# Kernel optimization log

Measured on AMD Instinct MI355X. Metric: run time of the kernel, lower is better.

The kernel has to match this reference:

```python
import jax, jax.numpy as jnp
import numpy as np

N = 20000       # num_nodes
E = 200000      # ~ N*N*0.0005 directed edges from erdos_renyi
IN = 64         # in_channels
HID = 128       # hidden_channels (per head)
H = 4           # heads
OUT = 10        # out_channels
K1 = 10000      # ceil(0.5*N) nodes kept by pool1 (single graph -> static)
K2 = 5000       # ceil(0.5*K1) kept by pool2
NEG_SLOPE = 0.2 # PyG GATConv default negative_slope


def setup_inputs() -> dict:
    key = jax.random.key(0)
    ks = jax.random.split(key, 16)
    def glorot(k, shp, fan):
        return (jax.random.normal(k, shp, jnp.float32) / np.sqrt(fan)).astype(jnp.float32)
    x = jax.random.normal(ks[0], (N, IN), jnp.float32)
    edge_index = jax.random.randint(ks[1], (2, E), 0, N, dtype=jnp.int32)
    batch = jnp.zeros((N,), jnp.int32)
    W1 = glorot(ks[2], (IN, H * HID), IN)
    a_src1 = glorot(ks[3], (H, HID), HID)
    a_dst1 = glorot(ks[4], (H, HID), HID)
    b1 = jnp.zeros((H * HID,), jnp.float32)
    pw1 = glorot(ks[5], (H * HID,), H * HID)
    W2 = glorot(ks[6], (H * HID, H * HID), H * HID)
    a_src2 = glorot(ks[7], (H, HID), HID)
    a_dst2 = glorot(ks[8], (H, HID), HID)
    b2 = jnp.zeros((H * HID,), jnp.float32)
    pw2 = glorot(ks[9], (H * HID,), H * HID)
    Wl = glorot(ks[10], (H * HID, OUT), H * HID)
    bl = jnp.zeros((OUT,), jnp.float32)
    return dict(x=x, edge_index=edge_index, batch=batch,
                W1=W1, a_src1=a_src1, a_dst1=a_dst1, b1=b1, pw1=pw1,
                W2=W2, a_src2=a_src2, a_dst2=a_dst2, b2=b2, pw2=pw2,
                Wl=Wl, bl=bl)


def _gat(x, src, dst, emask, W, a_src, a_dst, bias):
    """PyG GATConv: gather -> LeakyReLU edge score -> scatter-softmax over dst -> scatter-add.
    Self-loops added (PyG default). emask marks valid edges (invalid edges point at node 0)."""
    n = x.shape[0]
    Hh, C = a_src.shape
    h = (x @ W).reshape(n, Hh, C)                      # [n,H,C]
    asrc = jnp.einsum('nhc,hc->nh', h, a_src)          # [n,H]
    adst = jnp.einsum('nhc,hc->nh', h, a_dst)
    loops = jnp.arange(n, dtype=src.dtype)
    sa = jnp.concatenate([src, loops])                 # [E+n]
    da = jnp.concatenate([dst, loops])
    ma = jnp.concatenate([emask, jnp.ones((n,), bool)])
    logit = jax.nn.leaky_relu(asrc[sa] + adst[da], negative_slope=NEG_SLOPE)  # [E+n,H]
    logit = jnp.where(ma[:, None], logit, -1e9)
    mx = jax.ops.segment_max(logit, da, num_segments=n)        # every node has a self-loop
    e = jnp.where(ma[:, None], jnp.exp(logit - mx[da]), 0.0)
    den = jax.ops.segment_sum(e, da, num_segments=n)
    alpha = e / den[da]                                         # [E+n,H]
    msg = (alpha[:, :, None] * h[sa]).reshape(-1, Hh * C)       # [E+n,H*C]
    return jax.ops.segment_sum(msg, da, num_segments=n) + bias  # concat heads + bias


def _topk_pool(x, src, dst, emask, w, k):
    """PyG TopKPooling (single graph): score = tanh(x.w/||w||), keep top-k nodes,
    scale kept features by score, relabel & mask edges between kept nodes."""
    score = jnp.tanh((x @ w) / jnp.linalg.norm(w))     # [n]
    vals, perm = jax.lax.top_k(score, k)
    xn = x[perm] * vals[:, None]                       # [k,F]
    remap = jnp.full((x.shape[0],), -1, jnp.int32).at[perm].set(jnp.arange(k, dtype=jnp.int32))
    s2 = remap[src]
    d2 = remap[dst]
    m2 = emask & (s2 >= 0) & (d2 >= 0)
    return xn, jnp.where(m2, s2, 0), jnp.where(m2, d2, 0), m2


def reference(x, edge_index, batch, W1, a_src1, a_dst1, b1, pw1,
              W2, a_src2, a_dst2, b2, pw2, Wl, bl):
    src = edge_index[0]
    dst = edge_index[1]
    mask = jnp.ones((src.shape[0],), bool)
    h = jax.nn.elu(_gat(x, src, dst, mask, W1, a_src1, a_dst1, b1))
    h, src, dst, mask = _topk_pool(h, src, dst, mask, pw1, K1)
    h = jax.nn.elu(_gat(h, src, dst, mask, W2, a_src2, a_dst2, b2))
    h, src, dst, mask = _topk_pool(h, src, dst, mask, pw2, K2)
    g = jnp.mean(h, axis=0, keepdims=True)             # global_mean_pool, single graph
    return g @ Wl + bl                                  # [1, OUT]
```

## Files before the change

kernel.cpp:

```cpp
#include <hip/hip_runtime.h>
#include <math.h>

#define N_NODES 20000
#define E_EDGES 200000
#define K1_KEEP 10000
#define K2_KEEP 5000
#define HIDC 128
#define NHEAD 4
#define FDIM 512
#define NEG 0.2f
#define BSTRIDE 64
#define SELCAP 20
#define MPAD 10112
#define MPAD1 20096
#define FR_GRID 250
#define FR_RPB 40

typedef _Float16 half8 __attribute__((ext_vector_type(8)));
typedef _Float16 half4 __attribute__((ext_vector_type(4)));
typedef float f32x4 __attribute__((ext_vector_type(4)));

__device__ __forceinline__ float leaky(float x){ return x > 0.f ? x : NEG * x; }
__device__ __forceinline__ float elu(float x){ return x > 0.f ? x : expm1f(x); }
__device__ __forceinline__ unsigned ordkey(float f){
    unsigned u = __float_as_uint(f);
    return (u & 0x80000000u) ? ~u : (u | 0x80000000u);
}

__global__ __launch_bounds__(256) void prep_x(const float* __restrict__ x,
        _Float16* __restrict__ X0, _Float16* __restrict__ X1)
{
    int tid = blockIdx.x * 256 + threadIdx.x;
    int r = tid >> 3, c8 = (tid & 7) << 3;
    half8 v0 = (half8)0, v1 = (half8)0;
    if (r < N_NODES){
        const float4* p = reinterpret_cast<const float4*>(&x[(size_t)r * 64 + c8]);
        float4 x0 = p[0], x1 = p[1];
        float vals[8] = {x0.x, x0.y, x0.z, x0.w, x1.x, x1.y, x1.z, x1.w};
#pragma unroll
        for (int j = 0; j < 8; ++j){
            _Float16 h = (_Float16)vals[j];
            v0[j] = h;
            v1[j] = (_Float16)(vals[j] - (float)h);
        }
    }
    *reinterpret_cast<half8*>(&X0[(size_t)r * 64 + c8]) = v0;
    *reinterpret_cast<half8*>(&X1[(size_t)r * 64 + c8]) = v1;
}

__global__ __launch_bounds__(256) void prep_w1x(const float* __restrict__ W1,
        _Float16* __restrict__ B0, _Float16* __restrict__ B1,
        int* __restrict__ ctmp, int cn,
        const float* __restrict__ cw, float* __restrict__ cinvn)
{
    int bid = blockIdx.x;
    int t = threadIdx.x;
    if (bid < 32){
        __shared__ float tile[32][33];
        int bn = bid & 15, bk = bid >> 4;
        int n0 = bn * 32, k0 = bk * 32;
        int j = t & 31, i0 = t >> 5;
#pragma unroll
        for (int ii = 0; ii < 32; ii += 8)
            tile[i0 + ii][j] = W1[(size_t)(k0 + i0 + ii) * 512 + n0 + j];
        __syncthreads();
#pragma unroll
        for (int ii = 0; ii < 32; ii += 8){
            float v = tile[j][i0 + ii];
            _Float16 h0 = (_Float16)v;
            _Float16 h1 = (_Float16)(v - (float)h0);
            size_t o = (size_t)(n0 + i0 + ii) * 64 + k0 + j;
            B0[o] = h0; B1[o] = h1;
        }
    } else if (bid < 32 + 79){
        int i = (bid - 32) * 256 + t;
        if (i < cn) ctmp[i] = 0;
    } else {
        __shared__ float redc[4];
        float s = cw[t] * cw[t] + cw[t + 256] * cw[t + 256];
#pragma unroll
        for (int off = 32; off > 0; off >>= 1) s += __shfl_xor(s, off);
        if ((t & 63) == 0) redc[t >> 6] = s;
        __syncthreads();
        if (t == 0) *cinvn = rsqrtf(redc[0] + redc[1] + redc[2] + redc[3]);
    }
}

__global__ __launch_bounds__(256) void prep_w2(const float* __restrict__ W2,
        _Float16* __restrict__ B0, _Float16* __restrict__ B1)
{
    __shared__ float tile[32][33];
    int bn = blockIdx.x & 15, bk = blockIdx.x >> 4;
    int n0 = bn * 32, k0 = bk * 32;
    int t = threadIdx.x;
    int j = t & 31, i0 = t >> 5;
#pragma unroll
    for (int ii = 0; ii < 32; ii += 8)
        tile[i0 + ii][j] = W2[(size_t)(k0 + i0 + ii) * 512 + n0 + j];
    __syncthreads();
#pragma unroll
    for (int ii = 0; ii < 32; ii += 8){
        float v = tile[j][i0 + ii];
        _Float16 h0 = (_Float16)v;
        _Float16 h1 = (_Float16)(v - (float)h0);
        size_t o = (size_t)(n0 + i0 + ii) * 512 + k0 + j;
        B0[o] = h0; B1[o] = h1;
    }
}

__global__ __launch_bounds__(256) void prep_a(const float* __restrict__ out1,
        const int* __restrict__ oldi, const float* __restrict__ score,
        _Float16* __restrict__ A0, _Float16* __restrict__ A1)
{
    int tid = blockIdx.x * 256 + threadIdx.x;
    int r = tid >> 6, kq = (tid & 63) << 3;
    half8 v0 = (half8)0, v1 = (half8)0;
    if (r < K1_KEEP){
        int o = oldi[r];
        float sc = score[o];
        const float4* p = reinterpret_cast<const float4*>(&out1[(size_t)o * 512 + kq]);
        float4 x0 = p[0], x1 = p[1];
        float vals[8] = {x0.x, x0.y, x0.z, x0.w, x1.x, x1.y, x1.z, x1.w};
#pragma unroll
        for (int j = 0; j < 8; ++j){
            float v = vals[j] * sc;
            _Float16 h = (_Float16)v;
            v0[j] = h;
            v1[j] = (_Float16)(v - (float)h);
        }
    }
    *reinterpret_cast<half8*>(&A0[(size_t)r * 512 + kq]) = v0;
    *reinterpret_cast<half8*>(&A1[(size_t)r * 512 + kq]) = v1;
}

template<int KK>
__global__ __launch_bounds__(256, 2) void gemm_mfma(
        const _Float16* __restrict__ A0, const _Float16* __restrict__ A1,
        const _Float16* __restrict__ B0, const _Float16* __restrict__ B1,
        const float* __restrict__ avS, const float* __restrict__ avD,
        _Float16* __restrict__ C, float* __restrict__ asrc, float* __restrict__ adst,
        int nrows)
{
    __shared__ _Float16 smem[2][4][128][32];
    int t = threadIdx.x;
    int l = t & 63, w = t >> 6;
    int wr = w >> 1, wc = w & 1;
    int bidn = blockIdx.x & 3, bidm = blockIdx.x >> 2;
    int row0 = bidm * 128, col0 = bidn * 128;

    const _Float16* plane = (w == 0) ? A0 : (w == 1) ? A1 : (w == 2) ? B0 : B1;
    int prow0 = (w < 2) ? row0 : col0;
    int mloc = l >> 2;
    int gsw = (l & 3) ^ (mloc & 3);
    const _Float16* gbase = plane + (size_t)(prow0 + mloc) * KK + gsw * 8;

    f32x4 acc[4][4];
#pragma unroll
    for (int m = 0; m < 4; ++m)
#pragma unroll
        for (int n = 0; n < 4; ++n) acc[m][n] = (f32x4){0.f, 0.f, 0.f, 0.f};

    auto stage = [&](int buf, int chunk){
        const _Float16* src = gbase + chunk * 32;
        char* db = (char*)&smem[buf][w][0][0];
#pragma unroll
        for (int i = 0; i < 8; ++i)
            __builtin_amdgcn_global_load_lds(
                (const __attribute__((address_space(1))) void*)(src + (size_t)i * (KK * 16)),
                (__attribute__((address_space(3))) void*)(db + i * 1024), 16, 0, 0);
    };

    int rb = (l & 15) * 64 + (((l >> 4) ^ (l & 3)) * 16);
    const char* sb = (const char*)smem;

    constexpr int NCH = KK / 32;
    stage(0, 0);
    __syncthreads();
    for (int c = 0; c < NCH; ++c){
        int buf = c & 1;
        if (c < NCH - 1) stage(buf ^ 1, c + 1);
        const char* base = sb + buf * 32768;
        half8 a0[4], a1[4], b0[4], b1[4];
#pragma unroll
        for (int m = 0; m < 4; ++m){
            a0[m] = *(const half8*)(base +         wr * 4096 + m * 1024 + rb);
            a1[m] = *(const half8*)(base +  8192 + wr * 4096 + m * 1024 + rb);
            b0[m] = *(const half8*)(base + 16384 + wc * 4096 + m * 1024 + rb);
            b1[m] = *(const half8*)(base + 24576 + wc * 4096 + m * 1024 + rb);
        }
#pragma unroll
        for (int m = 0; m < 4; ++m)
#pragma unroll
            for (int n = 0; n < 4; ++n)
                acc[m][n] = __builtin_amdgcn_mfma_f32_16x16x32_f16(a0[m], b0[n], acc[m][n], 0, 0, 0);
#pragma unroll
        for (int m = 0; m < 4; ++m)
#pragma unroll
            for (int n = 0; n < 4; ++n)
                acc[m][n] = __builtin_amdgcn_mfma_f32_16x16x32_f16(a0[m], b1[n], acc[m][n], 0, 0, 0);
#pragma unroll
        for (int m = 0; m < 4; ++m)
#pragma unroll
            for (int n = 0; n < 4; ++n)
                acc[m][n] = __builtin_amdgcn_mfma_f32_16x16x32_f16(a1[m], b0[n], acc[m][n], 0, 0, 0);
        __syncthreads();
    }

    int head = bidn;
    const float* asv = avS + head * HIDC + wc * 64;
    const float* adv = avD + head * HIDC + wc * 64;
    int lc = l & 15, lg = l >> 4;
    int rbase = row0 + wr * 64;
    int cbase = col0 + wc * 64;
#pragma unroll
    for (int m = 0; m < 4; ++m){
#pragma unroll
        for (int q = 0; q < 4; ++q){
            int row = rbase + m * 16 + lg * 4 + q;
            bool ok = row < nrows;
            float s = 0.f, d = 0.f;
#pragma unroll
            for (int n = 0; n < 4; ++n){
                float v = acc[m][n][q];
                int cc = n * 16 + lc;
                if (ok) C[(size_t)row * 512 + cbase + cc] = (_Float16)v;
                s += v * asv[cc];
                d += v * adv[cc];
            }
#pragma unroll
            for (int off = 1; off < 16; off <<= 1){
                s += __shfl_xor(s, off);
                d += __shfl_xor(d, off);
            }
            if (ok && lc == 0){
                asrc[row * 8 + head * 2 + wc] = s;
                adst[row * 8 + head * 2 + wc] = d;
            }
        }
    }
}

__global__ void edge_fill(const int* __restrict__ src, const int* __restrict__ dst, int e,
                          int* __restrict__ tmp, int* __restrict__ csr){
    int i = blockIdx.x * 256 + threadIdx.x;
    if (i >= e) return;
    int d = dst[i];
    int pos = atomicAdd(&tmp[d], 1);
    if (pos < BSTRIDE) csr[d * BSTRIDE + pos] = src[i];
}

template<bool FILTER>
__global__ __launch_bounds__(256) void gat_fused(const _Float16* __restrict__ h,
        const float* __restrict__ asrc, const float* __restrict__ adst,
        const int* __restrict__ degs, const int* __restrict__ csr,
        const int* __restrict__ oldi, const int* __restrict__ remap,
        const float* __restrict__ bias, const float* __restrict__ pw,
        const float* __restrict__ invn, float* __restrict__ out,
        float* __restrict__ score, int n)
{
    int node = blockIdx.x * 4 + (threadIdx.x >> 6);
    int lane = threadIdx.x & 63;
    if (node >= n) return;
    int od = FILTER ? oldi[node] : node;
    int deg = degs[od]; if (deg > BSTRIDE) deg = BSTRIDE;
    int e0 = od * BSTRIDE;
    int ph = lane & 3;
    int pe = lane >> 2;
    float adn, sown;
    {
        float2 dv = *reinterpret_cast<const float2*>(&adst[(size_t)node * 8 + ph * 2]);
        float2 sv = *reinterpret_cast<const float2*>(&asrc[(size_t)node * 8 + ph * 2]);
        adn = dv.x + dv.y; sown = sv.x + sv.y;
    }
    float slog = leaky(sown + adn);
    int sreg[4];
    float mx = slog;
#pragma unroll
    for (int blk = 0; blk < 4; ++blk){
        int j = blk * 16 + pe;
        int s = -1;
        if (j < deg){
            s = csr[e0 + j];
            if (FILTER) s = remap[s];
            if (s >= 0){
                float2 v = *reinterpret_cast<const float2*>(&asrc[(size_t)s * 8 + ph * 2]);
                mx = fmaxf(mx, leaky(v.x + v.y + adn));
            }
        }
        sreg[blk] = s;
    }
#pragma unroll
    for (int off = 4; off < 64; off <<= 1) mx = fmaxf(mx, __shfl_xor(mx, off));
    float aexp[4];
    float lsum = 0.f;
#pragma unroll
    for (int blk = 0; blk < 4; ++blk){
        float ex = 0.f;
        int s = sreg[blk];
        if (s >= 0){
            float2 v = *reinterpret_cast<const float2*>(&asrc[(size_t)s * 8 + ph * 2]);
            ex = expf(leaky(v.x + v.y + adn) - mx);
        }
        aexp[blk] = ex;
        lsum += ex;
    }
#pragma unroll
    for (int off = 4; off < 64; off <<= 1) lsum += __shfl_xor(lsum, off);
    float es  = expf(slog - mx);
    float inv = 1.f / (lsum + es);

    int f0 = lane * 8;
    int hf = lane >> 4;
    float invh  = __shfl(inv, hf);
    float aself = __shfl(es, hf) * invh;
    float4 acc0, acc1;
    {
        half8 v = *reinterpret_cast<const half8*>(&h[(size_t)node * FDIM + f0]);
        acc0 = make_float4(aself * (float)v[0], aself * (float)v[1],
                           aself * (float)v[2], aself * (float)v[3]);
        acc1 = make_float4(aself * (float)v[4], aself * (float)v[5],
                           aself * (float)v[6], aself * (float)v[7]);
    }
#pragma unroll
    for (int blk = 0; blk < 4; ++blk){
        int base = blk * 16;
        if (base >= deg) break;
        int cnt = deg - base; if (cnt > 16) cnt = 16;
        for (int e = 0; e < cnt; ++e){
            int s = __shfl(sreg[blk], e * 4);
            if (FILTER && s < 0) continue;
            float al = __shfl(aexp[blk], e * 4 + hf) * invh;
            half8 u = *reinterpret_cast<const half8*>(&h[(size_t)s * FDIM + f0]);
            acc0.x += al * (float)u[0]; acc0.y += al * (float)u[1];
            acc0.z += al * (float)u[2]; acc0.w += al * (float)u[3];
            acc1.x += al * (float)u[4]; acc1.y += al * (float)u[5];
            acc1.z += al * (float)u[6]; acc1.w += al * (float)u[7];
        }
    }
    const float4* bp = reinterpret_cast<const float4*>(&bias[f0]);
    float4 b0 = bp[0], b1 = bp[1];
    float4 o0 = make_float4(elu(acc0.x + b0.x), elu(acc0.y + b0.y),
                            elu(acc0.z + b0.z), elu(acc0.w + b0.w));
    float4 o1 = make_float4(elu(acc1.x + b1.x), elu(acc1.y + b1.y),
                            elu(acc1.z + b1.z), elu(acc1.w + b1.w));
    float4* op = reinterpret_cast<float4*>(&out[(size_t)node * FDIM + f0]);
    op[0] = o0; op[1] = o1;
    const float4* wp = reinterpret_cast<const float4*>(&pw[f0]);
    float4 w0 = wp[0], w1 = wp[1];
    float s = o0.x * w0.x + o0.y * w0.y + o0.z * w0.z + o0.w * w0.w
            + o1.x * w1.x + o1.y * w1.y + o1.z * w1.z + o1.w * w1.w;
#pragma unroll
    for (int off = 32; off > 0; off >>= 1) s += __shfl_xor(s, off);
    if (lane == 0) score[node] = tanhf(s * (*invn));
}

__global__ __launch_bounds__(1024) void select_compact(const float* __restrict__ score,
        int n, int k, int* __restrict__ remap, int* __restrict__ oldidx,
        float* __restrict__ zbuf, int zn,
        const float* __restrict__ w, float* __restrict__ invn)
{
    __shared__ unsigned hist[16][256];
    __shared__ unsigned wtot[4];
    __shared__ unsigned s_prefix, s_rem, l_tie, l_keep;
    __shared__ float red2[16];
    int t = threadIdx.x;
    int wv = t >> 6;
    unsigned keys[SELCAP];
#pragma unroll
    for (int j = 0; j < SELCAP; ++j){
        int i = t + j * 1024;
        keys[j] = (i < n) ? ordkey(score[i]) : 0u;
    }
    if (t == 0){ s_prefix = 0u; s_rem = (unsigned)k; l_tie = 0u; l_keep = 0u; }
    for (int i = t; i < 16 * 256; i += 1024) ((unsigned*)hist)[i] = 0u;
    if (zbuf && t < zn) zbuf[t] = 0.f;
    __syncthreads();
    for (int pass = 3; pass >= 0; --pass){
        unsigned shift = (unsigned)pass * 8u;
        unsigned pmask = (pass == 3) ? 0u : (0xFFFFFFFFu << (shift + 8u));
        unsigned pref = s_prefix;
        unsigned remv = s_rem;
#pragma unroll
        for (int j = 0; j < SELCAP; ++j){
            int i = t + j * 1024;
            if (i < n && (keys[j] & pmask) == pref)
                atomicAdd(&hist[wv][(keys[j] >> shift) & 255u], 1u);
        }
        __syncthreads();
        unsigned c = 0, v = 0;
        if (t < 256){
            unsigned a = 0;
#pragma unroll
            for (int wq = 0; wq < 16; ++wq) a += hist[wq][t];
            c = a; v = a;
#pragma unroll
            for (int off = 1; off < 64; off <<= 1){
                unsigned o = __shfl_down(v, off);
                if ((t & 63) + off < 64) v += o;
            }
            if ((t & 63) == 0) wtot[t >> 6] = v;
        }
        __syncthreads();
        if (t < 256){
#pragma unroll
            for (int q = 0; q < 4; ++q)
                if (q > (t >> 6)) v += wtot[q];
            unsigned nxt = v - c;
            if (v >= remv && nxt < remv){
                s_prefix = pref | ((unsigned)t << shift);
                s_rem = remv - nxt;
            }
        }
        __syncthreads();
        if (pass > 0){
            for (int i = t; i < 16 * 256; i += 1024) ((unsigned*)hist)[i] = 0u;
            __syncthreads();
        }
    }
    unsigned T = s_prefix, ties = s_rem;
#pragma unroll
    for (int j = 0; j < SELCAP; ++j){
        int i = t + j * 1024;
        if (i >= n) continue;
        unsigned key = keys[j];
        int keep = 0;
        if (key > T) keep = 1;
        else if (key == T){
            unsigned tk = atomicAdd(&l_tie, 1u);
            if (tk < ties) keep = 1;
        }
        if (keep){
            int pos = (int)atomicAdd(&l_keep, 1u);
            remap[i] = pos;
            oldidx[pos] = i;
        } else remap[i] = -1;
    }
    if (w){
        float s = (t < 512) ? w[t] * w[t] : 0.f;
#pragma unroll
        for (int off = 32; off > 0; off >>= 1) s += __shfl_xor(s, off);
        if ((t & 63) == 0) red2[wv] = s;
        __syncthreads();
        if (t == 0){
            float a = 0.f;
            for (int i = 0; i < 16; ++i) a += red2[i];
            *invn = rsqrtf(a);
        }
    }
}

__global__ __launch_bounds__(512) void final_reduce(const float* __restrict__ x,
        const int* __restrict__ remap, const float* __restrict__ score,
        float* __restrict__ acc, const float* __restrict__ Wl)
{
    __shared__ float gsh[512];
    int t = threadIdx.x;
    int r0 = blockIdx.x * FR_RPB;
    float a = 0.f;
#pragma unroll
    for (int i = 0; i < FR_RPB; i += 4){
        int rr = r0 + i;
        float s0 = (remap[rr + 0] >= 0) ? score[rr + 0] : 0.f;
        float s1 = (remap[rr + 1] >= 0) ? score[rr + 1] : 0.f;
        float s2 = (remap[rr + 2] >= 0) ? score[rr + 2] : 0.f;
        float s3 = (remap[rr + 3] >= 0) ? score[rr + 3] : 0.f;
        float v0 = x[(size_t)(rr + 0) * FDIM + t];
        float v1 = x[(size_t)(rr + 1) * FDIM + t];
        float v2 = x[(size_t)(rr + 2) * FDIM + t];
        float v3 = x[(size_t)(rr + 3) * FDIM + t];
        a += v0 * s0 + v1 * s1 + v2 * s2 + v3 * s3;
    }
    gsh[t] = a;
    __syncthreads();
    int wv = t >> 6, lane = t & 63;
#pragma unroll
    for (int rep = 0; rep < 2; ++rep){
        int w = wv + rep * 8;
        if (w >= 10) break;
        float s = 0.f;
#pragma unroll
        for (int f = 0; f < 8; ++f) s += gsh[lane + f * 64] * Wl[(lane + f * 64) * 10 + w];
#pragma unroll
        for (int off = 32; off > 0; off >>= 1) s += __shfl_xor(s, off);
        if (lane == 0) atomicAdd(&acc[w * 32], s);
    }
}

__global__ __launch_bounds__(64) void final_out(const float* __restrict__ acc,
        const float* __restrict__ bl, float* __restrict__ out)
{
    int t = threadIdx.x;
    if (t < 10) out[t] = acc[t * 32] * (1.0f / K2_KEEP) + bl[t];
}

extern "C" void kernel_launch(void* const* d_in, const int* in_sizes, int n_in,
                              void* d_out, int out_size, void* d_ws, size_t ws_size,
                              hipStream_t stream)
{
    (void)in_sizes; (void)n_in; (void)out_size; (void)ws_size;
    const float* x   = (const float*)d_in[0];
    const int*   ei  = (const int*)  d_in[1];
    const float* W1  = (const float*)d_in[3];
    const float* as1 = (const float*)d_in[4];
    const float* ad1 = (const float*)d_in[5];
    const float* b1  = (const float*)d_in[6];
    const float* pw1 = (const float*)d_in[7];
    const float* W2  = (const float*)d_in[8];
    const float* as2 = (const float*)d_in[9];
    const float* ad2 = (const float*)d_in[10];
    const float* b2  = (const float*)d_in[11];
    const float* pw2 = (const float*)d_in[12];
    const float* Wl  = (const float*)d_in[13];
    const float* bl  = (const float*)d_in[14];
    const int* src1 = ei;
    const int* dst1 = ei + E_EDGES;

    char* wsb = (char*)d_ws;
    size_t off = 0;
    auto alloc = [&](size_t bytes) -> char* {
        char* p = wsb + off;
        off += (bytes + 255) & ~(size_t)255;
        return p;
    };
    _Float16* h1f = (_Float16*)alloc((size_t)N_NODES * FDIM * 2);
    float* out1 = (float*)alloc((size_t)N_NODES * FDIM * 4);
    float* asrc = (float*)alloc((size_t)N_NODES * 8 * 4);
    float* adst = (float*)alloc((size_t)N_NODES * 8 * 4);
    float* score= (float*)alloc((size_t)N_NODES * 4);
    float* invn = (float*)alloc(4);
    int* tmp  = (int*)alloc((size_t)N_NODES * 4);
    int* csr  = (int*)alloc((size_t)N_NODES * BSTRIDE * 4);
    int* remap= (int*)alloc((size_t)N_NODES * 4);
    int* oldi = (int*)alloc((size_t)K1_KEEP * 4);
    float* racc = (float*)alloc(320 * 4);
    _Float16* a0p = (_Float16*)alloc((size_t)MPAD * FDIM * 2);
    _Float16* a1p = (_Float16*)alloc((size_t)MPAD * FDIM * 2);
    _Float16* w2t0 = (_Float16*)alloc((size_t)FDIM * FDIM * 2);
    _Float16* w2t1 = (_Float16*)alloc((size_t)FDIM * FDIM * 2);
    _Float16* x0p = (_Float16*)alloc((size_t)MPAD1 * 64 * 2);
    _Float16* x1p = (_Float16*)alloc((size_t)MPAD1 * 64 * 2);
    _Float16* w1t0 = (_Float16*)alloc((size_t)FDIM * 64 * 2);
    _Float16* w1t1 = (_Float16*)alloc((size_t)FDIM * 64 * 2);
    _Float16* h2f = h1f;
    float* out2 = out1;

    prep_x<<<MPAD1 * 8 / 256, 256, 0, stream>>>(x, x0p, x1p);
    prep_w1x<<<112, 256, 0, stream>>>(W1, w1t0, w1t1, tmp, N_NODES, pw1, invn);
    gemm_mfma<64><<<(MPAD1 / 128) * 4, 256, 0, stream>>>(x0p, x1p, w1t0, w1t1,
            as1, ad1, h1f, asrc, adst, N_NODES);
    prep_w2<<<256, 256, 0, stream>>>(W2, w2t0, w2t1);
    edge_fill<<<(E_EDGES + 255) / 256, 256, 0, stream>>>(src1, dst1, E_EDGES, tmp, csr);
    gat_fused<false><<<(N_NODES + 3) / 4, 256, 0, stream>>>(h1f, asrc, adst, tmp, csr,
            nullptr, nullptr, b1, pw1, invn, out1, score, N_NODES);

    select_compact<<<1, 1024, 0, stream>>>(score, N_NODES, K1_KEEP, remap, oldi,
                                           nullptr, 0, pw2, invn);

    prep_a<<<MPAD / 4, 256, 0, stream>>>(out1, oldi, score, a0p, a1p);
    gemm_mfma<512><<<(MPAD / 128) * 4, 256, 0, stream>>>(a0p, a1p, w2t0, w2t1,
            as2, ad2, h2f, asrc, adst, K1_KEEP);
    gat_fused<true><<<(K1_KEEP + 3) / 4, 256, 0, stream>>>(h2f, asrc, adst, tmp, csr,
            oldi, remap, b2, pw2, invn, out2, score, K1_KEEP);

    select_compact<<<1, 1024, 0, stream>>>(score, K1_KEEP, K2_KEEP, remap, oldi,
                                           racc, 320, nullptr, nullptr);
    final_reduce<<<FR_GRID, 512, 0, stream>>>(out2, remap, score, racc, Wl);
    final_out<<<1, 64, 0, stream>>>(racc, bl, (float*)d_out);
}
```

Measured before the change: 271.0 us.

## Split single-block top-k radix select into multi-block histogram, scan and compact kernels

Replaces the one-block, 1024-thread radix select with a grid-wide version: each of four byte passes runs a multi-block histogram kernel followed by a one-block scan kernel, and a final multi-block compaction uses prefix sums plus global atomics to assign positions. This spreads the selection across many CUs instead of serialising it on one, at the cost of nine launches per selection and round trips through global memory. Kept-node ordering changes from atomic order to block order; tie handling keeps an equivalent count.

```diff
diff --git a/kernel.cpp b/kernel.cpp
--- a/kernel.cpp
+++ b/kernel.cpp
@@ -10,11 +10,11 @@
 #define FDIM 512
 #define NEG 0.2f
 #define BSTRIDE 64
-#define SELCAP 20
 #define MPAD 10112
 #define MPAD1 20096
 #define FR_GRID 250
 #define FR_RPB 40
+#define SSTRIDE 16
 
 typedef _Float16 half8 __attribute__((ext_vector_type(8)));
 typedef _Float16 half4 __attribute__((ext_vector_type(4)));
@@ -354,98 +354,132 @@
     if (lane == 0) score[node] = tanhf(s * (*invn));
 }
 
-__global__ __launch_bounds__(1024) void select_compact(const float* __restrict__ score,
-        int n, int k, int* __restrict__ remap, int* __restrict__ oldidx,
+
+__global__ __launch_bounds__(1024) void sel_init(unsigned* __restrict__ gbins,
+                                                 unsigned* __restrict__ meta)
+{
+    int i = blockIdx.x * 1024 + threadIdx.x;
+    if (i < 256 * SSTRIDE) gbins[i] = 0u;
+    if (i < 64) meta[i] = 0u;
+}
+
+template<int PASS>
+__global__ __launch_bounds__(256) void sel_hist(const float* __restrict__ score,
+        int n, unsigned* __restrict__ gbins, const unsigned* __restrict__ meta)
+{
+    __shared__ unsigned h[4][256];
+    int t = threadIdx.x, wv = t >> 6;
+    for (int i = t; i < 1024; i += 256) ((unsigned*)h)[i] = 0u;
+    __syncthreads();
+    unsigned pref = 0u, pmask = 0u;
+    if (PASS < 3){ pref = meta[0]; pmask = 0xFFFFFFFFu << (PASS * 8 + 8); }
+    int base = blockIdx.x * 512 + t;
+#pragma unroll
+    for (int j = 0; j < 2; ++j){
+        int i = base + j * 256;
+        if (i < n){
+            unsigned key = ordkey(score[i]);
+            if ((key & pmask) == pref)
+                atomicAdd(&h[wv][(key >> (PASS * 8)) & 255u], 1u);
+        }
+    }
+    __syncthreads();
+    unsigned a = h[0][t] + h[1][t] + h[2][t] + h[3][t];
+    if (a) atomicAdd(&gbins[t * SSTRIDE], a);
+}
+
+__global__ __launch_bounds__(256) void sel_scan(unsigned* __restrict__ gbins,
+        unsigned* __restrict__ meta, int pass, unsigned k)
+{
+    __shared__ unsigned wt[4];
+    int t = threadIdx.x, lane = t & 63, wv = t >> 6;
+    unsigned c = gbins[t * SSTRIDE];
+    gbins[t * SSTRIDE] = 0u;
+    unsigned rem  = (pass == 3) ? k  : meta[1];
+    unsigned pref = (pass == 3) ? 0u : meta[0];
+    unsigned v = c;
+#pragma unroll
+    for (int off = 1; off < 64; off <<= 1){
+        unsigned o = __shfl_down(v, off);
+        if (lane + off < 64) v += o;
+    }
+    if (lane == 0) wt[wv] = v;
+    __syncthreads();
+#pragma unroll
+    for (int q = 0; q < 4; ++q)
+        if (q > wv) v += wt[q];
+    unsigned nxt = v - c;
+    if (v >= rem && nxt < rem){
+        meta[0] = pref | ((unsigned)t << (pass * 8));
+        meta[1] = rem - nxt;
+    }
+    if (pass == 0 && t == 0){ meta[16] = 0u; meta[32] = 0u; }
+}
+
+__global__ __launch_bounds__(256) void sel_compact(const float* __restrict__ score,
+        int n, int k, unsigned* __restrict__ meta,
+        int* __restrict__ remap, int* __restrict__ oldidx,
         float* __restrict__ zbuf, int zn,
         const float* __restrict__ w, float* __restrict__ invn)
 {
-    __shared__ unsigned hist[16][256];
-    __shared__ unsigned wtot[4];
-    __shared__ unsigned s_prefix, s_rem, l_tie, l_keep;
-    __shared__ float red2[16];
-    int t = threadIdx.x;
-    int wv = t >> 6;
-    unsigned keys[SELCAP];
-#pragma unroll
-    for (int j = 0; j < SELCAP; ++j){
-        int i = t + j * 1024;
-        keys[j] = (i < n) ? ordkey(score[i]) : 0u;
-    }
-    if (t == 0){ s_prefix = 0u; s_rem = (unsigned)k; l_tie = 0u; l_keep = 0u; }
-    for (int i = t; i < 16 * 256; i += 1024) ((unsigned*)hist)[i] = 0u;
-    if (zbuf && t < zn) zbuf[t] = 0.f;
-    __syncthreads();
-    for (int pass = 3; pass >= 0; --pass){
-        unsigned shift = (unsigned)pass * 8u;
-        unsigned pmask = (pass == 3) ? 0u : (0xFFFFFFFFu << (shift + 8u));
-        unsigned pref = s_prefix;
-        unsigned remv = s_rem;
-#pragma unroll
-        for (int j = 0; j < SELCAP; ++j){
-            int i = t + j * 1024;
-            if (i < n && (keys[j] & pmask) == pref)
-                atomicAdd(&hist[wv][(keys[j] >> shift) & 255u], 1u);
-        }
+    __shared__ unsigned wsum[4];
+    __shared__ unsigned gbaseS, tbaseS;
+    __shared__ float red2[4];
+    int t = threadIdx.x, lane = t & 63, wv = t >> 6;
+    unsigned T = meta[0], ties = meta[1];
+    int i0 = blockIdx.x * 512 + t;
+    int i1 = i0 + 256;
+    unsigned key0 = (i0 < n) ? ordkey(score[i0]) : 0u;
+    unsigned key1 = (i1 < n) ? ordkey(score[i1]) : 0u;
+    int g0 = (i0 < n && key0 > T) ? 1 : 0, e0 = (i0 < n && key0 == T) ? 1 : 0;
+    int g1 = (i1 < n && key1 > T) ? 1 : 0, e1 = (i1 < n && key1 == T) ? 1 : 0;
+    unsigned pk = ((unsigned)(g0 + g1) << 16) | (unsigned)(e0 + e1);
+    unsigned v = pk;
+#pragma unroll
+    for (int off = 1; off < 64; off <<= 1){
+        unsigned o = __shfl_up(v, off);
+        if (lane >= off) v += o;
+    }
+    if (lane == 63) wsum[wv] = v;
+    __syncthreads();
+    unsigned wb = 0;
+    for (int q = 0; q < wv; ++q) wb += wsum[q];
+    unsigned excl = wb + v - pk;
+    if (t == 255){
+        unsigned tot = wb + v;
+        gbaseS = atomicAdd(&meta[16], tot >> 16);
+        tbaseS = atomicAdd(&meta[32], tot & 0xFFFFu);
+    }
+    __syncthreads();
+    int gpos = (int)(gbaseS + (excl >> 16));
+    int tpos = (int)(tbaseS + (excl & 0xFFFFu));
+    int gtot = k - (int)ties;
+    if (i0 < n){
+        int pos = -1;
+        if (g0) pos = gpos;
+        else if (e0 && tpos < (int)ties) pos = gtot + tpos;
+        if (pos >= 0){ remap[i0] = pos; oldidx[pos] = i0; }
+        else remap[i0] = -1;
+    }
+    gpos += g0; tpos += e0;
+    if (i1 < n){
+        int pos = -1;
+        if (g1) pos = gpos;
+        else if (e1 && tpos < (int)ties) pos = gtot + tpos;
+        if (pos >= 0){ remap[i1] = pos; oldidx[pos] = i1; }
+        else remap[i1] = -1;
+    }
+    if (w && blockIdx.x == 0){
+        float s = w[t] * w[t] + w[t + 256] * w[t + 256];
+#pragma unroll
+        for (int off = 32; off > 0; off >>= 1) s += __shfl_xor(s, off);
+        if (lane == 0) red2[wv] = s;
         __syncthreads();
-        unsigned c = 0, v = 0;
-        if (t < 256){
-            unsigned a = 0;
-#pragma unroll
-            for (int wq = 0; wq < 16; ++wq) a += hist[wq][t];
-            c = a; v = a;
-#pragma unroll
-            for (int off = 1; off < 64; off <<= 1){
-                unsigned o = __shfl_down(v, off);
-                if ((t & 63) + off < 64) v += o;
-            }
-            if ((t & 63) == 0) wtot[t >> 6] = v;
-        }
-        __syncthreads();
-        if (t < 256){
-#pragma unroll
-            for (int q = 0; q < 4; ++q)
-                if (q > (t >> 6)) v += wtot[q];
-            unsigned nxt = v - c;
-            if (v >= remv && nxt < remv){
-                s_prefix = pref | ((unsigned)t << shift);
-                s_rem = remv - nxt;
-            }
-        }
-        __syncthreads();
-        if (pass > 0){
-            for (int i = t; i < 16 * 256; i += 1024) ((unsigned*)hist)[i] = 0u;
-            __syncthreads();
-        }
-    }
-    unsigned T = s_prefix, ties = s_rem;
-#pragma unroll
-    for (int j = 0; j < SELCAP; ++j){
-        int i = t + j * 1024;
-        if (i >= n) continue;
-        unsigned key = keys[j];
-        int keep = 0;
-        if (key > T) keep = 1;
-        else if (key == T){
-            unsigned tk = atomicAdd(&l_tie, 1u);
-            if (tk < ties) keep = 1;
-        }
-        if (keep){
-            int pos = (int)atomicAdd(&l_keep, 1u);
-            remap[i] = pos;
-            oldidx[pos] = i;
-        } else remap[i] = -1;
-    }
-    if (w){
-        float s = (t < 512) ? w[t] * w[t] : 0.f;
-#pragma unroll
-        for (int off = 32; off > 0; off >>= 1) s += __shfl_xor(s, off);
-        if ((t & 63) == 0) red2[wv] = s;
-        __syncthreads();
-        if (t == 0){
-            float a = 0.f;
-            for (int i = 0; i < 16; ++i) a += red2[i];
-            *invn = rsqrtf(a);
-        }
+        if (t == 0) *invn = rsqrtf(red2[0] + red2[1] + red2[2] + red2[3]);
+    }
+    if (zbuf && blockIdx.x == 0){
+        if (t < zn) zbuf[t] = 0.f;
+        if (t + 256 < zn) zbuf[t + 256] = 0.f;
     }
 }
 
@@ -491,6 +525,23 @@
 {
     int t = threadIdx.x;
     if (t < 10) out[t] = acc[t * 32] * (1.0f / K2_KEEP) + bl[t];
+}
+
+static inline void run_select(const float* score, int n, int k,
+        int* remap, int* oldi, unsigned* gbins, unsigned* meta,
+        float* zbuf, int zn, const float* w, float* invn, hipStream_t stream)
+{
+    int nb = (n + 511) / 512;
+    sel_hist<3><<<nb, 256, 0, stream>>>(score, n, gbins, meta);
+    sel_scan<<<1, 256, 0, stream>>>(gbins, meta, 3, (unsigned)k);
+    sel_hist<2><<<nb, 256, 0, stream>>>(score, n, gbins, meta);
+    sel_scan<<<1, 256, 0, stream>>>(gbins, meta, 2, (unsigned)k);
+    sel_hist<1><<<nb, 256, 0, stream>>>(score, n, gbins, meta);
+    sel_scan<<<1, 256, 0, stream>>>(gbins, meta, 1, (unsigned)k);
+    sel_hist<0><<<nb, 256, 0, stream>>>(score, n, gbins, meta);
+    sel_scan<<<1, 256, 0, stream>>>(gbins, meta, 0, (unsigned)k);
+    sel_compact<<<nb, 256, 0, stream>>>(score, n, k, meta, remap, oldi,
+                                        zbuf, zn, w, invn);
 }
 
 extern "C" void kernel_launch(void* const* d_in, const int* in_sizes, int n_in,
@@ -533,6 +584,8 @@
     int* remap= (int*)alloc((size_t)N_NODES * 4);
     int* oldi = (int*)alloc((size_t)K1_KEEP * 4);
     float* racc = (float*)alloc(320 * 4);
+    unsigned* gbins = (unsigned*)alloc(256 * SSTRIDE * 4);
+    unsigned* smeta = (unsigned*)alloc(64 * 4);
     _Float16* a0p = (_Float16*)alloc((size_t)MPAD * FDIM * 2);
     _Float16* a1p = (_Float16*)alloc((size_t)MPAD * FDIM * 2);
     _Float16* w2t0 = (_Float16*)alloc((size_t)FDIM * FDIM * 2);
@@ -544,6 +597,7 @@
     _Float16* h2f = h1f;
     float* out2 = out1;
 
+    sel_init<<<4, 1024, 0, stream>>>(gbins, smeta);
     prep_x<<<MPAD1 * 8 / 256, 256, 0, stream>>>(x, x0p, x1p);
     prep_w1x<<<112, 256, 0, stream>>>(W1, w1t0, w1t1, tmp, N_NODES, pw1, invn);
     gemm_mfma<64><<<(MPAD1 / 128) * 4, 256, 0, stream>>>(x0p, x1p, w1t0, w1t1,
@@ -553,8 +607,8 @@
     gat_fused<false><<<(N_NODES + 3) / 4, 256, 0, stream>>>(h1f, asrc, adst, tmp, csr,
             nullptr, nullptr, b1, pw1, invn, out1, score, N_NODES);
 
-    select_compact<<<1, 1024, 0, stream>>>(score, N_NODES, K1_KEEP, remap, oldi,
-                                           nullptr, 0, pw2, invn);
+    run_select(score, N_NODES, K1_KEEP, remap, oldi, gbins, smeta,
+               nullptr, 0, pw2, invn, stream);
 
     prep_a<<<MPAD / 4, 256, 0, stream>>>(out1, oldi, score, a0p, a1p);
     gemm_mfma<512><<<(MPAD / 128) * 4, 256, 0, stream>>>(a0p, a1p, w2t0, w2t1,
@@ -562,8 +616,8 @@
     gat_fused<true><<<(K1_KEEP + 3) / 4, 256, 0, stream>>>(h2f, asrc, adst, tmp, csr,
             oldi, remap, b2, pw2, invn, out2, score, K1_KEEP);
 
-    select_compact<<<1, 1024, 0, stream>>>(score, K1_KEEP, K2_KEEP, remap, oldi,
-                                           racc, 320, nullptr, nullptr);
+    run_select(score, K1_KEEP, K2_KEEP, remap, oldi, gbins, smeta,
+               racc, 320, nullptr, nullptr, stream);
     final_reduce<<<FR_GRID, 512, 0, stream>>>(out2, remap, score, racc, Wl);
     final_out<<<1, 64, 0, stream>>>(racc, bl, (float*)d_out);
 }
```

After: 274.5 us. No clear change (+1.3%).
